# Performance work log

Measured on AMD Instinct MI355X. Metric: run time of the kernel, lower is better.

## Reference

```python
import jax, jax.numpy as jnp
import numpy as np

DIM = 1024
HEADS = 16
DIM_HEAD = 64
INNER = HEADS * DIM_HEAD
SCALE = DIM_HEAD ** -0.5


def rotate_half(t):
    # '... (j d) -> ... j d' with j=2: split last dim in half
    x1, x2 = jnp.split(t, 2, axis=-1)
    return jnp.concatenate((-x2, x1), axis=-1)


def rotary_pos(n, d, dtype):
    inv_freq = 1.0 / (10000.0 ** (jnp.arange(0, d, 2, dtype=jnp.float32) / d))
    freqs = jnp.arange(n, dtype=jnp.float32)[:, None] * inv_freq[None, :]  # (n, d/2)
    return jnp.concatenate((freqs, freqs), axis=-1).astype(dtype)  # (n, d)


def apply_rope(pos, t):
    return t * jnp.cos(pos) + rotate_half(t) * jnp.sin(pos)


def setup_inputs() -> dict:
    key = jax.random.key(0)
    ks = jax.random.split(key, 5)
    x = jax.random.normal(ks[0], (2, 2048, DIM), dtype=jnp.float32)
    gamma = jnp.ones((DIM,), dtype=jnp.float32)
    beta = jnp.zeros((DIM,), dtype=jnp.float32)
    Wq = jax.random.normal(ks[1], (DIM, INNER), dtype=jnp.float32) * 0.02
    Wkv = jax.random.normal(ks[2], (DIM, 2 * INNER), dtype=jnp.float32) * 0.02
    Wo = jax.random.normal(ks[3], (INNER, DIM), dtype=jnp.float32) * 0.02
    return {"x": x, "gamma": gamma, "beta": beta, "Wq": Wq, "Wkv": Wkv, "Wo": Wo}


def reference(x, gamma, beta, Wq, Wkv, Wo):
    b, n, _ = x.shape
    # LayerNorm with learned gamma, fixed-zero beta buffer
    mu = jnp.mean(x, axis=-1, keepdims=True)
    var = jnp.var(x, axis=-1, keepdims=True)
    xn = (x - mu) / jnp.sqrt(var + 1e-5) * gamma + beta

    q = xn @ Wq                       # (b, n, inner)
    kv = xn @ Wkv
    k, v = jnp.split(kv, 2, axis=-1)

    def to_heads(t):
        return t.reshape(b, n, HEADS, DIM_HEAD).transpose(0, 2, 1, 3)  # b h n d

    q, k, v = map(to_heads, (q, k, v))

    pos = rotary_pos(n, DIM_HEAD, x.dtype)  # (n, d)
    q = apply_rope(pos, q)
    k = apply_rope(pos, k)

    q = q * SCALE
    sim = jnp.einsum('bhid,bhjd->bhij', q, k)

    neg = -jnp.finfo(sim.dtype).max
    causal_mask = jnp.triu(jnp.ones((n, n), dtype=bool), k=1)
    sim = jnp.where(causal_mask, neg, sim)

    attn = jax.nn.softmax(sim, axis=-1)
    out = jnp.einsum('bhij,bhjd->bhid', attn, v)
    out = out.transpose(0, 2, 1, 3).reshape(b, n, INNER)
    return out @ Wo
```

## Files before the change

kernel.cpp:

```cpp
#include <hip/hip_runtime.h>
#include <stdint.h>

typedef unsigned short u16;
typedef __attribute__((ext_vector_type(8))) short short8;
typedef __attribute__((ext_vector_type(4))) float floatx4;
typedef __attribute__((ext_vector_type(4))) unsigned short u16x4;
typedef __attribute__((ext_vector_type(2))) unsigned int uint2v;

__device__ __forceinline__ float bf2f(u16 v) {
  union { uint32_t u; float f; } x; x.u = ((uint32_t)v) << 16; return x.f;
}
__device__ __forceinline__ u16 f2bf(float f) {
  union { float f; uint32_t u; } x; x.f = f;
  uint32_t r = x.u + 0x7fffu + ((x.u >> 16) & 1u);
  return (u16)(r >> 16);
}
__device__ __forceinline__ uint32_t fu(float f) {
  union { float f; uint32_t u; } x; x.f = f; return x.u;
}

#define GL2LDS(g, l)                                                          \
  __builtin_amdgcn_global_load_lds(                                           \
      (const __attribute__((address_space(1))) void*)(g),                     \
      (__attribute__((address_space(3))) void*)(l), 16, 0, 0)

__global__ __launch_bounds__(256) void transpose_w_k(const float* __restrict__ in,
                                                     u16* __restrict__ out,
                                                     int R, int C) {
  __shared__ float tile[32][33];
  int c0 = blockIdx.x * 32, r0 = blockIdx.y * 32;
  int tx = threadIdx.x, ty = threadIdx.y;
#pragma unroll
  for (int i = 0; i < 32; i += 8)
    tile[ty + i][tx] = in[(size_t)(r0 + ty + i) * C + c0 + tx];
  __syncthreads();
#pragma unroll
  for (int i = 0; i < 32; i += 8)
    out[(size_t)(c0 + ty + i) * R + r0 + tx] = f2bf(tile[tx][ty + i]);
}

__global__ __launch_bounds__(256) void layernorm_k(const float* __restrict__ x,
                                                   const float* __restrict__ gamma,
                                                   const float* __restrict__ beta,
                                                   u16* __restrict__ xn) {
  int row = blockIdx.x;
  int t = threadIdx.x;
  const float* xr = x + (size_t)row * 1024;
  float4 xv = *(const float4*)(xr + t * 4);
  float v0 = xv.x, v1 = xv.y, v2 = xv.z, v3 = xv.w;
  float s = v0 + v1 + v2 + v3;
  float s2 = v0 * v0 + v1 * v1 + v2 * v2 + v3 * v3;
#pragma unroll
  for (int d = 1; d < 64; d <<= 1) {
    s += __shfl_xor(s, d, 64);
    s2 += __shfl_xor(s2, d, 64);
  }
  __shared__ float red[8];
  int lane = t & 63, wv = t >> 6;
  if (lane == 0) { red[wv] = s; red[4 + wv] = s2; }
  __syncthreads();
  s = red[0] + red[1] + red[2] + red[3];
  s2 = red[4] + red[5] + red[6] + red[7];
  float mu = s * (1.0f / 1024.0f);
  float var = s2 * (1.0f / 1024.0f) - mu * mu;
  float rstd = rsqrtf(var + 1e-5f);
  float4 gv = *(const float4*)(gamma + t * 4);
  float4 bv = *(const float4*)(beta + t * 4);
  u16x4 ov;
  ov.x = f2bf((v0 - mu) * rstd * gv.x + bv.x);
  ov.y = f2bf((v1 - mu) * rstd * gv.y + bv.y);
  ov.z = f2bf((v2 - mu) * rstd * gv.z + bv.z);
  ov.w = f2bf((v3 - mu) * rstd * gv.w + bv.w);
  *(u16x4*)(xn + (size_t)row * 1024 + t * 4) = ov;
}

__global__ __launch_bounds__(256) void gemm_bf16_k(const u16* __restrict__ A,
                                                   const u16* __restrict__ BT,
                                                   void* __restrict__ Cp,
                                                   int K, int lda, int ldc,
                                                   int f32out) {
  __shared__ __align__(16) u16 lA[128 * 32];
  __shared__ __align__(16) u16 lB[128 * 32];
  int tid = threadIdx.x;
  int bm = blockIdx.y * 128;
  int bn = blockIdx.x * 128;
  int w = tid >> 6, l = tid & 63;
  int wm = (w >> 1) * 64, wn = (w & 1) * 64;
  int lr = l & 15, lq = l >> 4;
  floatx4 acc[4][4] = {};
  int sr = w * 16 + (l >> 2);
  int sc = (l & 3) * 8;
  for (int k0 = 0; k0 < K; k0 += 32) {
    GL2LDS(A + (size_t)(bm + sr) * lda + k0 + sc, &lA[sr * 32 + sc]);
    GL2LDS(A + (size_t)(bm + sr + 64) * lda + k0 + sc, &lA[(sr + 64) * 32 + sc]);
    GL2LDS(BT + (size_t)(bn + sr) * K + k0 + sc, &lB[sr * 32 + sc]);
    GL2LDS(BT + (size_t)(bn + sr + 64) * K + k0 + sc, &lB[(sr + 64) * 32 + sc]);
    __syncthreads();
    short8 afr[4], bfr[4];
#pragma unroll
    for (int i = 0; i < 4; i++)
      afr[i] = *(const short8*)(&lA[(wm + i * 16 + lr) * 32 + lq * 8]);
#pragma unroll
    for (int i = 0; i < 4; i++)
      bfr[i] = *(const short8*)(&lB[(wn + i * 16 + lr) * 32 + lq * 8]);
#pragma unroll
    for (int mi = 0; mi < 4; mi++)
#pragma unroll
      for (int ni = 0; ni < 4; ni++)
        acc[mi][ni] = __builtin_amdgcn_mfma_f32_16x16x32_bf16(
            afr[mi], bfr[ni], acc[mi][ni], 0, 0, 0);
    __syncthreads();
  }
  if (f32out) {
    float* Cf = (float*)Cp;
#pragma unroll
    for (int mi = 0; mi < 4; mi++)
#pragma unroll
      for (int ni = 0; ni < 4; ni++)
#pragma unroll
        for (int r = 0; r < 4; r++) {
          int row = bm + wm + mi * 16 + lq * 4 + r;
          int col = bn + wn + ni * 16 + lr;
          Cf[(size_t)row * ldc + col] = acc[mi][ni][r];
        }
  } else {
    u16* Cb = (u16*)Cp;
#pragma unroll
    for (int mi = 0; mi < 4; mi++)
#pragma unroll
      for (int ni = 0; ni < 4; ni++)
#pragma unroll
        for (int r = 0; r < 4; r++) {
          int row = bm + wm + mi * 16 + lq * 4 + r;
          int col = bn + wn + ni * 16 + lr;
          Cb[(size_t)row * ldc + col] = f2bf(acc[mi][ni][r]);
        }
  }
}

__global__ __launch_bounds__(256) void gemm64_bf16_k(const u16* __restrict__ A,
                                                     const u16* __restrict__ BT,
                                                     float* __restrict__ C,
                                                     int K, int lda, int ldc) {
  __shared__ __align__(16) u16 lA[64 * 32];
  __shared__ __align__(16) u16 lB[128 * 32];
  int tid = threadIdx.x;
  int bm = blockIdx.y * 64;
  int bn = blockIdx.x * 128;
  int w = tid >> 6, l = tid & 63;
  int wm = (w >> 1) * 32, wn = (w & 1) * 64;
  int lr = l & 15, lq = l >> 4;
  floatx4 acc[2][4] = {};
  int sr = w * 16 + (l >> 2);
  int sc = (l & 3) * 8;
  for (int k0 = 0; k0 < K; k0 += 32) {
    GL2LDS(A + (size_t)(bm + sr) * lda + k0 + sc, &lA[sr * 32 + sc]);
    GL2LDS(BT + (size_t)(bn + sr) * K + k0 + sc, &lB[sr * 32 + sc]);
    GL2LDS(BT + (size_t)(bn + sr + 64) * K + k0 + sc, &lB[(sr + 64) * 32 + sc]);
    __syncthreads();
    short8 afr[2], bfr[4];
#pragma unroll
    for (int i = 0; i < 2; i++)
      afr[i] = *(const short8*)(&lA[(wm + i * 16 + lr) * 32 + lq * 8]);
#pragma unroll
    for (int i = 0; i < 4; i++)
      bfr[i] = *(const short8*)(&lB[(wn + i * 16 + lr) * 32 + lq * 8]);
#pragma unroll
    for (int mi = 0; mi < 2; mi++)
#pragma unroll
      for (int ni = 0; ni < 4; ni++)
        acc[mi][ni] = __builtin_amdgcn_mfma_f32_16x16x32_bf16(
            afr[mi], bfr[ni], acc[mi][ni], 0, 0, 0);
    __syncthreads();
  }
#pragma unroll
  for (int mi = 0; mi < 2; mi++)
#pragma unroll
    for (int ni = 0; ni < 4; ni++)
#pragma unroll
      for (int r = 0; r < 4; r++) {
        int row = bm + wm + mi * 16 + lq * 4 + r;
        int col = bn + wn + ni * 16 + lr;
        C[(size_t)row * ldc + col] = acc[mi][ni][r];
      }
}

__global__ __launch_bounds__(256) void rope_inplace_k(u16* __restrict__ qkv) {
  int idx = blockIdx.x * 256 + threadIdx.x;
  int ig = idx & 7;
  int h = (idx >> 3) & 15;
  int row = idx >> 7;
  int n = row & 2047;
  int i0 = ig * 4;
  const float QS = 0.125f * 1.44269504088896f;
  float c_[4], s_[4];
  float invf = exp2f(-(float)i0 * 0.4152410118609203f);
  const float rstep = 0.74989420933245582f;
#pragma unroll
  for (int e = 0; e < 4; e++) {
    float ang = (float)n * invf;
    c_[e] = cosf(ang);
    s_[e] = sinf(ang);
    invf *= rstep;
  }
  size_t base = (size_t)row * 3072 + h * 64 + i0;
  u16x4 qlo = *(u16x4*)(qkv + base);
  u16x4 qhi = *(u16x4*)(qkv + base + 32);
  u16x4 klo = *(u16x4*)(qkv + base + 1024);
  u16x4 khi = *(u16x4*)(qkv + base + 1056);
  u16x4 oqlo, oqhi, oklo, okhi;
#pragma unroll
  for (int e = 0; e < 4; e++) {
    float x1 = bf2f(((u16*)&qlo)[e]), x2 = bf2f(((u16*)&qhi)[e]);
    ((u16*)&oqlo)[e] = f2bf((x1 * c_[e] - x2 * s_[e]) * QS);
    ((u16*)&oqhi)[e] = f2bf((x2 * c_[e] + x1 * s_[e]) * QS);
    x1 = bf2f(((u16*)&klo)[e]); x2 = bf2f(((u16*)&khi)[e]);
    ((u16*)&oklo)[e] = f2bf(x1 * c_[e] - x2 * s_[e]);
    ((u16*)&okhi)[e] = f2bf(x2 * c_[e] + x1 * s_[e]);
  }
  *(u16x4*)(qkv + base) = oqlo;
  *(u16x4*)(qkv + base + 32) = oqhi;
  *(u16x4*)(qkv + base + 1024) = oklo;
  *(u16x4*)(qkv + base + 1056) = okhi;
}

__global__ __launch_bounds__(256) void transpose_v_k(const u16* __restrict__ qkv,
                                                     u16* __restrict__ vT) {
  __shared__ u16 tile[32][33];
  int bh = blockIdx.z;
  int b = bh >> 4, h = bh & 15;
  int n0 = blockIdx.x * 32, d0 = blockIdx.y * 32;
  int tx = threadIdx.x, ty = threadIdx.y;
#pragma unroll
  for (int i = 0; i < 32; i += 8)
    tile[ty + i][tx] =
        qkv[(size_t)(b * 2048 + n0 + ty + i) * 3072 + 2048 + h * 64 + d0 + tx];
  __syncthreads();
#pragma unroll
  for (int i = 0; i < 32; i += 8)
    vT[((size_t)bh * 64 + d0 + ty + i) * 2048 + n0 + tx] = tile[tx][ty + i];
}

#define LPT 72
__device__ __forceinline__ void attn_tile2(const u16* lK, const u16* lV, u16* lp,
                                           const short8* aq, floatx4* o,
                                           float& m_i, float& l_i, int lr, int lq,
                                           bool diag, int q0, int k0g,
                                           short8 ones) {
  floatx4 s[4];
#pragma unroll
  for (int ni = 0; ni < 4; ni++) {
    floatx4 a = {};
#pragma unroll
    for (int kc = 0; kc < 2; kc++) {
      int R = ni * 16 + lr;
      int c8 = (kc * 4 + lq) ^ (R & 7);
      short8 kf = *(const short8*)&lK[R * 64 + c8 * 8];
      a = __builtin_amdgcn_mfma_f32_16x16x32_bf16(kf, aq[kc], a, 0, 0, 0);
    }
    s[ni] = a;
  }
  if (diag) {
    int qg = q0 + lr;
#pragma unroll
    for (int ni = 0; ni < 4; ni++)
#pragma unroll
      for (int r = 0; r < 4; r++) {
        int kg = k0g + ni * 16 + lq * 4 + r;
        if (kg > qg) s[ni][r] = -1e30f;
      }
  }
  float mx = fmaxf(fmaxf(s[0][0], s[0][1]), fmaxf(s[0][2], s[0][3]));
#pragma unroll
  for (int ni = 1; ni < 4; ni++)
    mx = fmaxf(mx, fmaxf(fmaxf(s[ni][0], s[ni][1]), fmaxf(s[ni][2], s[ni][3])));
  mx = fmaxf(mx, __shfl_xor(mx, 16, 64));
  mx = fmaxf(mx, __shfl_xor(mx, 32, 64));
  float mnew = fmaxf(m_i, mx);
  float alpha = exp2f(m_i - mnew);
  m_i = mnew;
#pragma unroll
  for (int ni = 0; ni < 4; ni++) {
    float p0 = exp2f(s[ni][0] - mnew), p1 = exp2f(s[ni][1] - mnew);
    float p2 = exp2f(s[ni][2] - mnew), p3 = exp2f(s[ni][3] - mnew);
    uint2v dw;
    dw.x = (fu(p0) >> 16) | (fu(p1) & 0xFFFF0000u);
    dw.y = (fu(p2) >> 16) | (fu(p3) & 0xFFFF0000u);
    *(uint2v*)&lp[lr * LPT + ni * 16 + lq * 4] = dw;
  }
  short8 pb0 = *(const short8*)&lp[lr * LPT + lq * 8];
  short8 pb1 = *(const short8*)&lp[lr * LPT + 32 + lq * 8];
  floatx4 z = {};
  z = __builtin_amdgcn_mfma_f32_16x16x32_bf16(ones, pb0, z, 0, 0, 0);
  z = __builtin_amdgcn_mfma_f32_16x16x32_bf16(ones, pb1, z, 0, 0, 0);
  l_i = l_i * alpha + z[0];
#pragma unroll
  for (int di = 0; di < 4; di++)
#pragma unroll
    for (int r = 0; r < 4; r++) o[di][r] *= alpha;
#pragma unroll
  for (int di = 0; di < 4; di++) {
    int R = di * 16 + lr;
    int c80 = lq ^ (R & 7);
    int c81 = (4 + lq) ^ (R & 7);
    short8 v0 = *(const short8*)&lV[R * 64 + c80 * 8];
    o[di] = __builtin_amdgcn_mfma_f32_16x16x32_bf16(v0, pb0, o[di], 0, 0, 0);
    short8 v1 = *(const short8*)&lV[R * 64 + c81 * 8];
    o[di] = __builtin_amdgcn_mfma_f32_16x16x32_bf16(v1, pb1, o[di], 0, 0, 0);
  }
}

__global__ __launch_bounds__(256) void attn_k(const u16* __restrict__ qkv,
                                              const u16* __restrict__ vt,
                                              u16* __restrict__ out) {
  __shared__ __align__(16) u16 lK[64 * 64];
  __shared__ __align__(16) u16 lV[64 * 64];
  __shared__ __align__(16) u16 lP[4][16 * LPT];
  int bh = blockIdx.y;
  int b = bh >> 4, h = bh & 15;
  int p = blockIdx.x;
  int jB = 31 - p;
  int tid = threadIdx.x;
  int w = tid >> 6, l = tid & 63;
  int lr = l & 15, lq = l >> 4;
  int q0A = p * 64 + w * 16;
  int q0B = jB * 64 + w * 16;
  const u16* qb = qkv + (size_t)b * 2048 * 3072 + h * 64;
  const u16* kb = qkv + (size_t)b * 2048 * 3072 + 1024 + h * 64;
  const u16* vb = vt + (size_t)bh * 64 * 2048;
  short8 aqA[2], aqB[2];
  aqA[0] = *(const short8*)(qb + (size_t)(q0A + lr) * 3072 + lq * 8);
  aqA[1] = *(const short8*)(qb + (size_t)(q0A + lr) * 3072 + 32 + lq * 8);
  aqB[0] = *(const short8*)(qb + (size_t)(q0B + lr) * 3072 + lq * 8);
  aqB[1] = *(const short8*)(qb + (size_t)(q0B + lr) * 3072 + 32 + lq * 8);
  short8 ones;
#pragma unroll
  for (int i = 0; i < 8; i++) ones[i] = (short)0x3F80;
  floatx4 oA[4] = {}, oB[4] = {};
  float mA = -1e30f, lA_ = 0.0f, mB = -1e30f, lB_ = 0.0f;
  int srow8 = l >> 3;
  int sc8 = (l & 7) ^ srow8;
  u16* lp = &lP[w][0];
  for (int kt = 0; kt <= jB; ++kt) {
#pragma unroll
    for (int c = 0; c < 2; c++) {
      int m = w + c * 4;
      int row = m * 8 + srow8;
      GL2LDS(kb + (size_t)(kt * 64 + row) * 3072 + sc8 * 8, &lK[m * 512]);
      GL2LDS(vb + (size_t)row * 2048 + kt * 64 + sc8 * 8, &lV[m * 512]);
    }
    __syncthreads();
    attn_tile2(lK, lV, lp, aqB, oB, mB, lB_, lr, lq, kt == jB, q0B, kt * 64, ones);
    if (kt <= p)
      attn_tile2(lK, lV, lp, aqA, oA, mA, lA_, lr, lq, kt == p, q0A, kt * 64, ones);
    __syncthreads();
  }
  float rlA = 1.0f / lA_, rlB = 1.0f / lB_;
#pragma unroll
  for (int di = 0; di < 4; di++) {
    uint2v dwA, dwB;
    u16 a0 = f2bf(oA[di][0] * rlA), a1 = f2bf(oA[di][1] * rlA);
    u16 a2 = f2bf(oA[di][2] * rlA), a3 = f2bf(oA[di][3] * rlA);
    dwA.x = (uint32_t)a0 | ((uint32_t)a1 << 16);
    dwA.y = (uint32_t)a2 | ((uint32_t)a3 << 16);
    u16 b0 = f2bf(oB[di][0] * rlB), b1 = f2bf(oB[di][1] * rlB);
    u16 b2 = f2bf(oB[di][2] * rlB), b3 = f2bf(oB[di][3] * rlB);
    dwB.x = (uint32_t)b0 | ((uint32_t)b1 << 16);
    dwB.y = (uint32_t)b2 | ((uint32_t)b3 << 16);
    int dcol = h * 64 + di * 16 + lq * 4;
    *(uint2v*)(out + ((size_t)(b * 2048 + q0A + lr)) * 3072 + dcol) = dwA;
    *(uint2v*)(out + ((size_t)(b * 2048 + q0B + lr)) * 3072 + dcol) = dwB;
  }
}

extern "C" void kernel_launch(void* const* d_in, const int* in_sizes, int n_in,
                              void* d_out, int out_size, void* d_ws, size_t ws_size,
                              hipStream_t stream) {
  const float* x = (const float*)d_in[0];
  const float* gamma = (const float*)d_in[1];
  const float* beta = (const float*)d_in[2];
  const float* Wq = (const float*)d_in[3];
  const float* Wkv = (const float*)d_in[4];
  const float* Wo = (const float*)d_in[5];
  float* out = (float*)d_out;
  char* ws = (char*)d_ws;

  u16* qkv = (u16*)(ws);
  u16* wqkvT = (u16*)(ws + 25165824);
  u16* woT = (u16*)(ws + 31457280);
  u16* xn = (u16*)(ws + 33554432);
  u16* vT = xn;
  u16* attn_out = qkv + 2048;

  dim3 tb32(32, 8);
  transpose_w_k<<<dim3(32, 32), tb32, 0, stream>>>(Wq, wqkvT, 1024, 1024);
  transpose_w_k<<<dim3(64, 32), tb32, 0, stream>>>(Wkv, wqkvT + 1024 * 1024, 1024, 2048);
  transpose_w_k<<<dim3(32, 32), tb32, 0, stream>>>(Wo, woT, 1024, 1024);
  layernorm_k<<<4096, 256, 0, stream>>>(x, gamma, beta, xn);
  gemm_bf16_k<<<dim3(24, 32), 256, 0, stream>>>(xn, wqkvT, qkv, 1024, 1024, 3072, 0);
  rope_inplace_k<<<2048, 256, 0, stream>>>(qkv);
  transpose_v_k<<<dim3(64, 2, 32), tb32, 0, stream>>>(qkv, vT);
  attn_k<<<dim3(16, 32), 256, 0, stream>>>(qkv, vT, attn_out);
  gemm64_bf16_k<<<dim3(8, 64), 256, 0, stream>>>(attn_out, woT, out, 1024, 3072, 1024);
}
```

Before: 218.1 us.

## Double-buffer K/V tiles in attention, merge weight transposes, use perm packing

The attention kernel now keeps two LDS buffers for K and V and issues the async global-to-LDS load for the next key tile before computing on the current one. This hides load latency and drops one barrier per iteration. The three weight-transpose launches are merged into one 3D-grid launch, with blocks returning early when out of range. The bf16 packing of softmax probabilities uses a single byte-permute instruction instead of shift/mask/or. The extra LDS raises per-block shared memory and may lower occupancy. The single remaining barrier relies on the prefetch target buffer no longer being read by the previous iteration.

Result: no change. 214.3 us (-1.7%).

```diff
diff --git a/kernel.cpp b/kernel.cpp
--- a/kernel.cpp
+++ b/kernel.cpp
@@ -24,11 +24,18 @@
       (const __attribute__((address_space(1))) void*)(g),                     \
       (__attribute__((address_space(3))) void*)(l), 16, 0, 0)
 
-__global__ __launch_bounds__(256) void transpose_w_k(const float* __restrict__ in,
-                                                     u16* __restrict__ out,
-                                                     int R, int C) {
+__global__ __launch_bounds__(256) void transpose_w3_k(const float* __restrict__ Wq,
+                                                      const float* __restrict__ Wkv,
+                                                      const float* __restrict__ Wo,
+                                                      u16* __restrict__ wqkvT,
+                                                      u16* __restrict__ woT) {
   __shared__ float tile[32][33];
+  int z = blockIdx.z;
+  const float* in = (z == 0) ? Wq : (z == 1) ? Wkv : Wo;
+  u16* out = (z == 0) ? wqkvT : (z == 1) ? (wqkvT + 1024 * 1024) : woT;
+  int C = (z == 1) ? 2048 : 1024;
   int c0 = blockIdx.x * 32, r0 = blockIdx.y * 32;
+  if (c0 >= C) return;
   int tx = threadIdx.x, ty = threadIdx.y;
 #pragma unroll
   for (int i = 0; i < 32; i += 8)
@@ -36,7 +43,7 @@
   __syncthreads();
 #pragma unroll
   for (int i = 0; i < 32; i += 8)
-    out[(size_t)(c0 + ty + i) * R + r0 + tx] = f2bf(tile[tx][ty + i]);
+    out[(size_t)(c0 + ty + i) * 1024 + r0 + tx] = f2bf(tile[tx][ty + i]);
 }
 
 __global__ __launch_bounds__(256) void layernorm_k(const float* __restrict__ x,
@@ -284,8 +291,8 @@
     float p0 = exp2f(s[ni][0] - mnew), p1 = exp2f(s[ni][1] - mnew);
     float p2 = exp2f(s[ni][2] - mnew), p3 = exp2f(s[ni][3] - mnew);
     uint2v dw;
-    dw.x = (fu(p0) >> 16) | (fu(p1) & 0xFFFF0000u);
-    dw.y = (fu(p2) >> 16) | (fu(p3) & 0xFFFF0000u);
+    dw.x = __builtin_amdgcn_perm(fu(p1), fu(p0), 0x07060302u);
+    dw.y = __builtin_amdgcn_perm(fu(p3), fu(p2), 0x07060302u);
     *(uint2v*)&lp[lr * LPT + ni * 16 + lq * 4] = dw;
   }
   short8 pb0 = *(const short8*)&lp[lr * LPT + lq * 8];
@@ -313,8 +320,8 @@
 __global__ __launch_bounds__(256) void attn_k(const u16* __restrict__ qkv,
                                               const u16* __restrict__ vt,
                                               u16* __restrict__ out) {
-  __shared__ __align__(16) u16 lK[64 * 64];
-  __shared__ __align__(16) u16 lV[64 * 64];
+  __shared__ __align__(16) u16 lK[2][64 * 64];
+  __shared__ __align__(16) u16 lV[2][64 * 64];
   __shared__ __align__(16) u16 lP[4][16 * LPT];
   int bh = blockIdx.y;
   int b = bh >> 4, h = bh & 15;
@@ -341,19 +348,25 @@
   int srow8 = l >> 3;
   int sc8 = (l & 7) ^ srow8;
   u16* lp = &lP[w][0];
-  for (int kt = 0; kt <= jB; ++kt) {
+  auto stage = [&](int bufi, int kt) {
 #pragma unroll
     for (int c = 0; c < 2; c++) {
       int m = w + c * 4;
       int row = m * 8 + srow8;
-      GL2LDS(kb + (size_t)(kt * 64 + row) * 3072 + sc8 * 8, &lK[m * 512]);
-      GL2LDS(vb + (size_t)row * 2048 + kt * 64 + sc8 * 8, &lV[m * 512]);
+      GL2LDS(kb + (size_t)(kt * 64 + row) * 3072 + sc8 * 8, &lK[bufi][m * 512]);
+      GL2LDS(vb + (size_t)row * 2048 + kt * 64 + sc8 * 8, &lV[bufi][m * 512]);
     }
+  };
+  stage(0, 0);
+  for (int kt = 0; kt <= jB; ++kt) {
+    int cur = kt & 1;
     __syncthreads();
-    attn_tile2(lK, lV, lp, aqB, oB, mB, lB_, lr, lq, kt == jB, q0B, kt * 64, ones);
+    if (kt < jB) stage(cur ^ 1, kt + 1);
+    attn_tile2(lK[cur], lV[cur], lp, aqB, oB, mB, lB_, lr, lq, kt == jB, q0B,
+               kt * 64, ones);
     if (kt <= p)
-      attn_tile2(lK, lV, lp, aqA, oA, mA, lA_, lr, lq, kt == p, q0A, kt * 64, ones);
-    __syncthreads();
+      attn_tile2(lK[cur], lV[cur], lp, aqA, oA, mA, lA_, lr, lq, kt == p, q0A,
+                 kt * 64, ones);
   }
   float rlA = 1.0f / lA_, rlB = 1.0f / lB_;
 #pragma unroll
@@ -393,9 +406,7 @@
   u16* attn_out = qkv + 2048;
 
   dim3 tb32(32, 8);
-  transpose_w_k<<<dim3(32, 32), tb32, 0, stream>>>(Wq, wqkvT, 1024, 1024);
-  transpose_w_k<<<dim3(64, 32), tb32, 0, stream>>>(Wkv, wqkvT + 1024 * 1024, 1024, 2048);
-  transpose_w_k<<<dim3(32, 32), tb32, 0, stream>>>(Wo, woT, 1024, 1024);
+  transpose_w3_k<<<dim3(64, 32, 3), tb32, 0, stream>>>(Wq, Wkv, Wo, wqkvT, woT);
   layernorm_k<<<4096, 256, 0, stream>>>(x, gamma, beta, xn);
   gemm_bf16_k<<<dim3(24, 32), 256, 0, stream>>>(xn, wqkvT, qkv, 1024, 1024, 3072, 0);
   rope_inplace_k<<<2048, 256, 0, stream>>>(qkv);
```
